# Optimization experiments

Hardware: AMD Instinct MI355X
Metric: run time of the kernel (lower is better)

Reference implementation:

```python
import jax, jax.numpy as jnp
import numpy as np

EMBED = 768
HEADS = 12


def setup_inputs() -> dict:
    key = jax.random.key(0)
    k1, k2, k3 = jax.random.split(key, 3)
    B, N, E = 2, 2048, EMBED
    x = jax.random.normal(k1, (B, N, E), dtype=jnp.float32)
    w_qkv = jax.random.normal(k2, (3 * E, E), dtype=jnp.float32) * (1.0 / np.sqrt(E))
    b_qkv = jnp.zeros((3 * E,), dtype=jnp.float32)
    w_o = jax.random.normal(k3, (E, E), dtype=jnp.float32) * (1.0 / np.sqrt(E))
    b_o = jnp.zeros((E,), dtype=jnp.float32)
    return {"x": x, "w_qkv": w_qkv, "b_qkv": b_qkv, "w_o": w_o, "b_o": b_o}


def reference(x, w_qkv, b_qkv, w_o, b_o):
    B, N, E = x.shape
    H = HEADS
    d = E // H
    # fused qkv projection (torch Linear: x @ W^T + b)
    qkv = x @ w_qkv.T + b_qkv                       # [B, N, 3E]
    # Rearrange 'b n (h qkv e) -> b qkv h n e'
    qkv = qkv.reshape(B, N, H, 3, d).transpose(0, 3, 2, 1, 4)  # [B, 3, H, N, d]
    q, k, v = qkv[:, 0], qkv[:, 1], qkv[:, 2]       # each [B, H, N, d]
    scores = jnp.einsum("bhqd,bhkd->bhqk", q, k)    # [B, H, N, N]
    attn = jax.nn.softmax(scores / jnp.sqrt(jnp.float32(E)), axis=-1)
    ctx = jnp.einsum("bhqk,bhkd->bhqd", attn, v)    # [B, H, N, d]
    ctx = ctx.transpose(0, 2, 1, 3).reshape(B, N, E)  # 'b h n d -> b n (h d)'
    out = ctx @ w_o.T + b_o
    return out
```

## Files before the change

### kernel.cpp

```cpp
#include <hip/hip_runtime.h>

#define BB 2
#define NN 2048
#define EE 768
#define HH 12
#define DD 64
#define MM (BB*NN)
#define E3 (3*EE)
#define NSPLIT 2
#define KEYS_PER_SPLIT (NN/NSPLIT)
#define QSCALE 0.05205877280961602f

typedef __bf16 bf16x8 __attribute__((ext_vector_type(8)));
typedef float  f32x4  __attribute__((ext_vector_type(4)));
typedef unsigned short u16x8 __attribute__((ext_vector_type(8)));

#define MFMA(a,b,c) __builtin_amdgcn_mfma_f32_16x16x32_bf16(a,b,c,0,0,0)

__device__ __forceinline__ unsigned short f2bf(float f) {
    unsigned int u = __float_as_uint(f);
    u += 0x7FFFu + ((u >> 16) & 1u);
    return (unsigned short)(u >> 16);
}

__device__ __forceinline__ bf16x8 as_bf16x8(u16x8 v) {
    union { u16x8 u; bf16x8 b; } c; c.u = v; return c.b;
}

typedef __attribute__((address_space(3))) unsigned int as3u32;
typedef __attribute__((address_space(1))) unsigned int as1u32;
__device__ __forceinline__ void gll16(const void* g, void* l) {
    __builtin_amdgcn_global_load_lds((const as1u32*)(uintptr_t)g,
                                     (as3u32*)(unsigned int)(uintptr_t)l, 16, 0, 0);
}

#define XB4 786432
#define WQ4 442368
#define WO4 147456
__global__ __launch_bounds__(256)
void cast3(const float* __restrict__ x, const float* __restrict__ wq,
           const float* __restrict__ wo, unsigned short* __restrict__ dst) {
    int i = blockIdx.x * 256 + threadIdx.x;
    const float* src;
    int off;
    if (i < XB4)            { src = x;  off = i; }
    else if (i < XB4+WQ4)   { src = wq; off = i - XB4; }
    else                    { src = wo; off = i - XB4 - WQ4; }
    float4 v = ((const float4*)src)[off];
    ushort4 o;
    o.x = f2bf(v.x); o.y = f2bf(v.y); o.z = f2bf(v.z); o.w = f2bf(v.w);
    ((ushort4*)dst)[i] = o;
}

__global__ __launch_bounds__(256)
void gemm_qkv(const unsigned short* __restrict__ A, const unsigned short* __restrict__ W,
              const float* __restrict__ bias,
              unsigned short* __restrict__ o0, unsigned short* __restrict__ o1,
              unsigned short* __restrict__ o2)
{
    __shared__ unsigned short As[2][128 * 32];
    __shared__ unsigned short Bs[2][64 * 32];

    const int tid = threadIdx.x;
    const int l = tid & 63;
    const int w = tid >> 6;
    const int m0 = blockIdx.x * 128;
    const int c0 = blockIdx.y * 64;
    const int wm = (w >> 1) * 64;
    const int wn = (w & 1) * 32;

    const unsigned short* s_src[3];
    int s_off[3]; bool s_isA[3];
    #pragma unroll
    for (int s = 0; s < 3; ++s) {
        const int ch = 3*w + s;
        if (ch < 8) {
            s_src[s] = A + (size_t)(m0 + ch*16 + (l>>2)) * EE + (l&3)*8;
            s_off[s] = ch*512; s_isA[s] = true;
        } else {
            s_src[s] = W + (size_t)(c0 + (ch-8)*16 + (l>>2)) * EE + (l&3)*8;
            s_off[s] = (ch-8)*512; s_isA[s] = false;
        }
    }

    const f32x4 zero4 = {0.f, 0.f, 0.f, 0.f};
    f32x4 acc[4][2];
    #pragma unroll
    for (int i = 0; i < 4; ++i)
        #pragma unroll
        for (int j = 0; j < 2; ++j) acc[i][j] = zero4;

    auto stage = [&](unsigned short* aB, unsigned short* bB, int k0) {
        #pragma unroll
        for (int s = 0; s < 3; ++s)
            gll16(s_src[s] + k0, (s_isA[s] ? aB : bB) + s_off[s]);
    };
    auto compute = [&](const unsigned short* aB, const unsigned short* bB) {
        bf16x8 af[4], bf[2];
        #pragma unroll
        for (int i = 0; i < 4; ++i)
            af[i] = *(const bf16x8*)&aB[(wm + 16*i + (l&15))*32 + (l>>4)*8];
        #pragma unroll
        for (int j = 0; j < 2; ++j)
            bf[j] = *(const bf16x8*)&bB[(wn + 16*j + (l&15))*32 + (l>>4)*8];
        #pragma unroll
        for (int i = 0; i < 4; ++i)
            #pragma unroll
            for (int j = 0; j < 2; ++j)
                acc[i][j] = MFMA(af[i], bf[j], acc[i][j]);
    };

    stage(As[0], Bs[0], 0);
    asm volatile("s_waitcnt vmcnt(0)" ::: "memory");
    __builtin_amdgcn_s_barrier();

    for (int k0 = 0; k0 < EE; k0 += 64) {
        stage(As[1], Bs[1], k0 + 32);
        compute(As[0], Bs[0]);
        asm volatile("s_waitcnt vmcnt(0)" ::: "memory");
        __builtin_amdgcn_s_barrier();
        if (k0 + 64 < EE) stage(As[0], Bs[0], k0 + 64);
        compute(As[1], Bs[1]);
        asm volatile("s_waitcnt vmcnt(0)" ::: "memory");
        __builtin_amdgcn_s_barrier();
    }

    const int sec = c0 >> 6;
    const int hh = sec / 3;
    const int tt = sec - hh*3;
    #pragma unroll
    for (int j = 0; j < 2; ++j) {
        const int col = c0 + wn + 16*j + (l&15);
        const int dcol = wn + 16*j + (l&15);
        const float bj = bias[col];
        #pragma unroll
        for (int i = 0; i < 4; ++i) {
            const int row0 = m0 + wm + 16*i + (l>>4)*4;
            const int b = row0 >> 11;
            const int n = row0 & (NN - 1);
            if (tt == 2) {
                ushort4 pk;
                pk.x = f2bf(acc[i][j][0] + bj);
                pk.y = f2bf(acc[i][j][1] + bj);
                pk.z = f2bf(acc[i][j][2] + bj);
                pk.w = f2bf(acc[i][j][3] + bj);
                *(ushort4*)&o2[(((size_t)b*HH + hh)*DD + dcol)*NN + n] = pk;
            } else {
                unsigned short* dst = (tt == 0) ? o0 : o1;
                #pragma unroll
                for (int r = 0; r < 4; ++r) {
                    float val = acc[i][j][r] + bj;
                    if (tt == 0) val *= QSCALE;
                    dst[(((size_t)b*HH + hh)*NN + n + r)*DD + dcol] = f2bf(val);
                }
            }
        }
    }
}

__global__ __launch_bounds__(256)
void gemm_out(const unsigned short* __restrict__ A, const unsigned short* __restrict__ W,
              const float* __restrict__ bias, float* __restrict__ of)
{
    __shared__ unsigned short As[2][64 * 32];
    __shared__ unsigned short Bs[2][64 * 32];

    const int tid = threadIdx.x;
    const int l = tid & 63;
    const int w = tid >> 6;
    const int m0 = blockIdx.x * 64;
    const int c0 = blockIdx.y * 64;
    const int wm = (w >> 1) * 32;
    const int wn = (w & 1) * 32;

    const unsigned short* s_src[2];
    int s_off[2]; bool s_isA[2];
    #pragma unroll
    for (int s = 0; s < 2; ++s) {
        const int ch = 2*w + s;
        if (ch < 4) {
            s_src[s] = A + (size_t)(m0 + ch*16 + (l>>2)) * EE + (l&3)*8;
            s_off[s] = ch*512; s_isA[s] = true;
        } else {
            s_src[s] = W + (size_t)(c0 + (ch-4)*16 + (l>>2)) * EE + (l&3)*8;
            s_off[s] = (ch-4)*512; s_isA[s] = false;
        }
    }

    const f32x4 zero4 = {0.f, 0.f, 0.f, 0.f};
    f32x4 acc[2][2];
    #pragma unroll
    for (int i = 0; i < 2; ++i)
        #pragma unroll
        for (int j = 0; j < 2; ++j) acc[i][j] = zero4;

    auto stage = [&](unsigned short* aB, unsigned short* bB, int k0) {
        #pragma unroll
        for (int s = 0; s < 2; ++s)
            gll16(s_src[s] + k0, (s_isA[s] ? aB : bB) + s_off[s]);
    };
    auto compute = [&](const unsigned short* aB, const unsigned short* bB) {
        bf16x8 af[2], bf[2];
        #pragma unroll
        for (int i = 0; i < 2; ++i)
            af[i] = *(const bf16x8*)&aB[(wm + 16*i + (l&15))*32 + (l>>4)*8];
        #pragma unroll
        for (int j = 0; j < 2; ++j)
            bf[j] = *(const bf16x8*)&bB[(wn + 16*j + (l&15))*32 + (l>>4)*8];
        #pragma unroll
        for (int i = 0; i < 2; ++i)
            #pragma unroll
            for (int j = 0; j < 2; ++j)
                acc[i][j] = MFMA(af[i], bf[j], acc[i][j]);
    };

    stage(As[0], Bs[0], 0);
    asm volatile("s_waitcnt vmcnt(0)" ::: "memory");
    __builtin_amdgcn_s_barrier();

    for (int k0 = 0; k0 < EE; k0 += 64) {
        stage(As[1], Bs[1], k0 + 32);
        compute(As[0], Bs[0]);
        asm volatile("s_waitcnt vmcnt(0)" ::: "memory");
        __builtin_amdgcn_s_barrier();
        if (k0 + 64 < EE) stage(As[0], Bs[0], k0 + 64);
        compute(As[1], Bs[1]);
        asm volatile("s_waitcnt vmcnt(0)" ::: "memory");
        __builtin_amdgcn_s_barrier();
    }

    #pragma unroll
    for (int j = 0; j < 2; ++j) {
        const int col = c0 + wn + 16*j + (l&15);
        const float bj = bias[col];
        #pragma unroll
        for (int i = 0; i < 2; ++i) {
            #pragma unroll
            for (int r = 0; r < 4; ++r) {
                const int row = m0 + wm + 16*i + (l>>4)*4 + r;
                of[(size_t)row * EE + col] = acc[i][j][r] + bj;
            }
        }
    }
}

struct KVT { u16x8 k0, k1, k2, k3, v0, v1, v2, v3; };

__global__ __launch_bounds__(256)
void attn_mfma(const unsigned short* __restrict__ Q, const unsigned short* __restrict__ K,
               const unsigned short* __restrict__ Vt_g,
               float* __restrict__ Opart, float* __restrict__ Lpart)
{
    __shared__ unsigned short Ks[2 * 64 * 64];
    __shared__ unsigned short Vt[2 * 64 * 64];

    const int tid = threadIdx.x;
    const int l = tid & 63;
    const int w = tid >> 6;
    const int quad = l >> 4;
    const int lc = l & 15;
    const int x7 = lc & 7;

    const int id = blockIdx.x;
    const int sp = blockIdx.y;
    const int bh = id % 24;
    const int bq = id / 24;
    const size_t hb = (size_t)bh * NN * DD;

    const f32x4 zero4 = {0.f, 0.f, 0.f, 0.f};

    const int qrow = bq*64 + w*16 + lc;
    const bf16x8 qf0 = *(const bf16x8*)(Q + hb + (size_t)qrow*DD +      quad*8);
    const bf16x8 qf1 = *(const bf16x8*)(Q + hb + (size_t)qrow*DD + 32 + quad*8);

    f32x4 o[4];
    #pragma unroll
    for (int dj = 0; dj < 4; ++dj) o[dj] = zero4;
    float lsum = 0.f;

    const int srow = tid >> 2;
    const int sc = tid & 3;
    const unsigned short* kbase = K + hb + (size_t)(sp*KEYS_PER_SPLIT + srow)*DD + sc*16;
    const int keyA = (sc & 1)*8 + (sc >> 1)*32;
    const unsigned short* vbase = Vt_g + hb + (size_t)srow*NN + sp*KEYS_PER_SPLIT + keyA;
    const int c0s = ((2*sc)     ^ (srow & 7)) * 8;
    const int c1s = ((2*sc + 1) ^ (srow & 7)) * 8;
    const int so = srow * 64;

    const int chq0 = ((    quad) ^ x7) * 8;
    const int chq1 = ((4 + quad) ^ x7) * 8;

    auto loadt = [&](KVT& R, int kt) {
        const unsigned short* k0p = kbase + (size_t)kt*128*DD;
        const unsigned short* v0p = vbase + kt*128;
        R.k0 = *(const u16x8*)k0p;
        R.k1 = *(const u16x8*)(k0p + 8);
        R.k2 = *(const u16x8*)(k0p + (size_t)64*DD);
        R.k3 = *(const u16x8*)(k0p + (size_t)64*DD + 8);
        R.v0 = *(const u16x8*)v0p;
        R.v1 = *(const u16x8*)(v0p + 16);
        R.v2 = *(const u16x8*)(v0p + 64);
        R.v3 = *(const u16x8*)(v0p + 64 + 16);
    };

    auto step = [&](KVT& CUR, KVT& NXT, int kt) {
        asm volatile("s_waitcnt lgkmcnt(0)" ::: "memory");
        __builtin_amdgcn_s_barrier();

        u16x8 w0 = __builtin_shufflevector(CUR.v0, CUR.v1, 0,1,2,3, 8,9,10,11);
        u16x8 w1 = __builtin_shufflevector(CUR.v0, CUR.v1, 4,5,6,7, 12,13,14,15);
        u16x8 w2 = __builtin_shufflevector(CUR.v2, CUR.v3, 0,1,2,3, 8,9,10,11);
        u16x8 w3 = __builtin_shufflevector(CUR.v2, CUR.v3, 4,5,6,7, 12,13,14,15);
        *(u16x8*)&Ks[so + c0s]        = CUR.k0;
        *(u16x8*)&Ks[so + c1s]        = CUR.k1;
        *(u16x8*)&Ks[4096 + so + c0s] = CUR.k2;
        *(u16x8*)&Ks[4096 + so + c1s] = CUR.k3;
        *(u16x8*)&Vt[so + c0s]        = w0;
        *(u16x8*)&Vt[so + c1s]        = w1;
        *(u16x8*)&Vt[4096 + so + c0s] = w2;
        *(u16x8*)&Vt[4096 + so + c1s] = w3;

        if (kt + 1 < KEYS_PER_SPLIT/128) loadt(NXT, kt + 1);

        asm volatile("s_waitcnt lgkmcnt(0)" ::: "memory");
        __builtin_amdgcn_s_barrier();
        __builtin_amdgcn_sched_barrier(0);

        #pragma unroll
        for (int hf = 0; hf < 2; ++hf) {
            const int base = hf * 4096;

            f32x4 st[4];
            #pragma unroll
            for (int jf = 0; jf < 4; ++jf) {
                bf16x8 kf0 = *(const bf16x8*)&Ks[base + (16*jf + lc)*64 + chq0];
                bf16x8 kf1 = *(const bf16x8*)&Ks[base + (16*jf + lc)*64 + chq1];
                f32x4 acc0 = MFMA(kf0, qf0, zero4);
                st[jf] = MFMA(kf1, qf1, acc0);
            }

            f32x4 ev[4];
            #pragma unroll
            for (int jf = 0; jf < 4; ++jf) {
                ev[jf][0] = __builtin_amdgcn_exp2f(st[jf][0]);
                ev[jf][1] = __builtin_amdgcn_exp2f(st[jf][1]);
                ev[jf][2] = __builtin_amdgcn_exp2f(st[jf][2]);
                ev[jf][3] = __builtin_amdgcn_exp2f(st[jf][3]);
                lsum += (ev[jf][0] + ev[jf][1]) + (ev[jf][2] + ev[jf][3]);
            }
            u16x8 p0, p1;
            #pragma unroll
            for (int r = 0; r < 4; ++r) {
                p0[r]     = f2bf(ev[0][r]);
                p0[r + 4] = f2bf(ev[1][r]);
                p1[r]     = f2bf(ev[2][r]);
                p1[r + 4] = f2bf(ev[3][r]);
            }
            const bf16x8 pf0 = as_bf16x8(p0);
            const bf16x8 pf1 = as_bf16x8(p1);

            #pragma unroll
            for (int dj = 0; dj < 4; ++dj) {
                bf16x8 vf0 = *(const bf16x8*)&Vt[base + (16*dj + lc)*64 + chq0];
                bf16x8 vf1 = *(const bf16x8*)&Vt[base + (16*dj + lc)*64 + chq1];
                o[dj] = MFMA(vf0, pf0, o[dj]);
                o[dj] = MFMA(vf1, pf1, o[dj]);
            }
        }
    };

    KVT ra, rb;
    loadt(ra, 0);
    for (int it = 0; it < KEYS_PER_SPLIT/256; ++it) {
        step(ra, rb, 2*it);
        step(rb, ra, 2*it + 1);
    }

    lsum += __shfl_xor(lsum, 16);
    lsum += __shfl_xor(lsum, 32);

    const int n = bq*64 + w*16 + lc;
    float* op = Opart + ((size_t)(sp*24 + bh)*NN + n)*DD + quad*4;
    #pragma unroll
    for (int dj = 0; dj < 4; ++dj)
        *(f32x4*)(op + 16*dj) = o[dj];
    if (quad == 0)
        Lpart[(size_t)(sp*24 + bh)*NN + n] = lsum;
}

#define RTOT (24*NN)
__global__ __launch_bounds__(256)
void combine(const float* __restrict__ Op, const float* __restrict__ Lp,
             unsigned short* __restrict__ ctx)
{
    const int t = blockIdx.x * 256 + threadIdx.x;
    const int r = t >> 4;
    const int c = t & 15;
    const float4 a = *(const float4*)&Op[(size_t)r*DD + c*4];
    const float4 bv = *(const float4*)&Op[((size_t)RTOT + r)*DD + c*4];
    const float inv = 1.f / (Lp[r] + Lp[RTOT + r]);
    const int bh = r >> 11;
    const int n = r & (NN - 1);
    const int b = bh / 12;
    const int h = bh - b*12;
    ushort4 pk;
    pk.x = f2bf((a.x + bv.x) * inv);
    pk.y = f2bf((a.y + bv.y) * inv);
    pk.z = f2bf((a.z + bv.z) * inv);
    pk.w = f2bf((a.w + bv.w) * inv);
    *(ushort4*)&ctx[((size_t)(b*NN + n))*EE + h*DD + c*4] = pk;
}

extern "C" void kernel_launch(void* const* d_in, const int* in_sizes, int n_in,
                              void* d_out, int out_size, void* d_ws, size_t ws_size,
                              hipStream_t stream)
{
    const float* x     = (const float*)d_in[0];
    const float* w_qkv = (const float*)d_in[1];
    const float* b_qkv = (const float*)d_in[2];
    const float* w_o   = (const float*)d_in[3];
    const float* b_o   = (const float*)d_in[4];
    float* out = (float*)d_out;

    unsigned short* wsu = (unsigned short*)d_ws;
    const size_t XB = (size_t)MM * EE;
    const size_t WQ = (size_t)E3 * EE;
    const size_t WO = (size_t)EE * EE;
    const size_t HS = (size_t)BB * HH * NN * DD;
    unsigned short* xb   = wsu;
    unsigned short* wqb  = xb  + XB;
    unsigned short* wob  = wqb + WQ;
    unsigned short* qb   = wob + WO;
    unsigned short* kb   = qb  + HS;
    unsigned short* vtb  = kb  + HS;
    unsigned short* ctxb = vtb + HS;
    float* opart = (float*)(ctxb + HS);
    float* lpart = opart + (size_t)NSPLIT * 24 * NN * DD;

    cast3<<<(XB4 + WQ4 + WO4)/256, 256, 0, stream>>>(x, w_qkv, w_o, xb);

    dim3 g1(MM/128, E3/64);
    gemm_qkv<<<g1, 256, 0, stream>>>(xb, wqb, b_qkv, qb, kb, vtb);

    dim3 g2(768, NSPLIT);
    attn_mfma<<<g2, 256, 0, stream>>>(qb, kb, vtb, opart, lpart);

    combine<<<(RTOT*16)/256, 256, 0, stream>>>(opart, lpart, ctxb);

    dim3 g3(MM/64, EE/64);
    gemm_out<<<g3, 256, 0, stream>>>(ctxb, wob, b_o, out);
}
```

Baseline: 171.4 us.

## Load K and V fragments directly from global memory, dropping LDS staging

The attention kernel no longer stages K and V tiles through shared memory with double-buffered register prefetch and barriers. Each wave now reads its MFMA operand fragments straight from global memory (8-byte loads for V^T), assembles the V operand from four 4-element pieces, and drops all block-level synchronisation. This removes LDS traffic and barrier stalls, but each wave redundantly fetches the same K/V data through cache with smaller, less coalesced loads and no explicit prefetch overlap.

```diff
diff --git a/kernel.cpp b/kernel.cpp
--- a/kernel.cpp
+++ b/kernel.cpp
@@ -14,6 +14,7 @@
 typedef __bf16 bf16x8 __attribute__((ext_vector_type(8)));
 typedef float  f32x4  __attribute__((ext_vector_type(4)));
 typedef unsigned short u16x8 __attribute__((ext_vector_type(8)));
+typedef unsigned short u16x4 __attribute__((ext_vector_type(4)));
 
 #define MFMA(a,b,c) __builtin_amdgcn_mfma_f32_16x16x32_bf16(a,b,c,0,0,0)
 
@@ -25,6 +26,10 @@
 
 __device__ __forceinline__ bf16x8 as_bf16x8(u16x8 v) {
     union { u16x8 u; bf16x8 b; } c; c.u = v; return c.b;
+}
+
+__device__ __forceinline__ bf16x8 combine48(u16x4 a, u16x4 b) {
+    union { u16x4 q[2]; bf16x8 v; } c; c.q[0] = a; c.q[1] = b; return c.v;
 }
 
 typedef __attribute__((address_space(3))) unsigned int as3u32;
@@ -244,22 +249,16 @@
     }
 }
 
-struct KVT { u16x8 k0, k1, k2, k3, v0, v1, v2, v3; };
-
 __global__ __launch_bounds__(256)
 void attn_mfma(const unsigned short* __restrict__ Q, const unsigned short* __restrict__ K,
                const unsigned short* __restrict__ Vt_g,
                float* __restrict__ Opart, float* __restrict__ Lpart)
 {
-    __shared__ unsigned short Ks[2 * 64 * 64];
-    __shared__ unsigned short Vt[2 * 64 * 64];
-
     const int tid = threadIdx.x;
     const int l = tid & 63;
     const int w = tid >> 6;
     const int quad = l >> 4;
     const int lc = l & 15;
-    const int x7 = lc & 7;
 
     const int id = blockIdx.x;
     const int sp = blockIdx.y;
@@ -278,102 +277,57 @@
     for (int dj = 0; dj < 4; ++dj) o[dj] = zero4;
     float lsum = 0.f;
 
-    const int srow = tid >> 2;
-    const int sc = tid & 3;
-    const unsigned short* kbase = K + hb + (size_t)(sp*KEYS_PER_SPLIT + srow)*DD + sc*16;
-    const int keyA = (sc & 1)*8 + (sc >> 1)*32;
-    const unsigned short* vbase = Vt_g + hb + (size_t)srow*NN + sp*KEYS_PER_SPLIT + keyA;
-    const int c0s = ((2*sc)     ^ (srow & 7)) * 8;
-    const int c1s = ((2*sc + 1) ^ (srow & 7)) * 8;
-    const int so = srow * 64;
-
-    const int chq0 = ((    quad) ^ x7) * 8;
-    const int chq1 = ((4 + quad) ^ x7) * 8;
-
-    auto loadt = [&](KVT& R, int kt) {
-        const unsigned short* k0p = kbase + (size_t)kt*128*DD;
-        const unsigned short* v0p = vbase + kt*128;
-        R.k0 = *(const u16x8*)k0p;
-        R.k1 = *(const u16x8*)(k0p + 8);
-        R.k2 = *(const u16x8*)(k0p + (size_t)64*DD);
-        R.k3 = *(const u16x8*)(k0p + (size_t)64*DD + 8);
-        R.v0 = *(const u16x8*)v0p;
-        R.v1 = *(const u16x8*)(v0p + 16);
-        R.v2 = *(const u16x8*)(v0p + 64);
-        R.v3 = *(const u16x8*)(v0p + 64 + 16);
-    };
-
-    auto step = [&](KVT& CUR, KVT& NXT, int kt) {
-        asm volatile("s_waitcnt lgkmcnt(0)" ::: "memory");
-        __builtin_amdgcn_s_barrier();
-
-        u16x8 w0 = __builtin_shufflevector(CUR.v0, CUR.v1, 0,1,2,3, 8,9,10,11);
-        u16x8 w1 = __builtin_shufflevector(CUR.v0, CUR.v1, 4,5,6,7, 12,13,14,15);
-        u16x8 w2 = __builtin_shufflevector(CUR.v2, CUR.v3, 0,1,2,3, 8,9,10,11);
-        u16x8 w3 = __builtin_shufflevector(CUR.v2, CUR.v3, 4,5,6,7, 12,13,14,15);
-        *(u16x8*)&Ks[so + c0s]        = CUR.k0;
-        *(u16x8*)&Ks[so + c1s]        = CUR.k1;
-        *(u16x8*)&Ks[4096 + so + c0s] = CUR.k2;
-        *(u16x8*)&Ks[4096 + so + c1s] = CUR.k3;
-        *(u16x8*)&Vt[so + c0s]        = w0;
-        *(u16x8*)&Vt[so + c1s]        = w1;
-        *(u16x8*)&Vt[4096 + so + c0s] = w2;
-        *(u16x8*)&Vt[4096 + so + c1s] = w3;
-
-        if (kt + 1 < KEYS_PER_SPLIT/128) loadt(NXT, kt + 1);
-
-        asm volatile("s_waitcnt lgkmcnt(0)" ::: "memory");
-        __builtin_amdgcn_s_barrier();
-        __builtin_amdgcn_sched_barrier(0);
-
-        #pragma unroll
-        for (int hf = 0; hf < 2; ++hf) {
-            const int base = hf * 4096;
-
-            f32x4 st[4];
-            #pragma unroll
-            for (int jf = 0; jf < 4; ++jf) {
-                bf16x8 kf0 = *(const bf16x8*)&Ks[base + (16*jf + lc)*64 + chq0];
-                bf16x8 kf1 = *(const bf16x8*)&Ks[base + (16*jf + lc)*64 + chq1];
-                f32x4 acc0 = MFMA(kf0, qf0, zero4);
-                st[jf] = MFMA(kf1, qf1, acc0);
-            }
-
-            f32x4 ev[4];
-            #pragma unroll
-            for (int jf = 0; jf < 4; ++jf) {
-                ev[jf][0] = __builtin_amdgcn_exp2f(st[jf][0]);
-                ev[jf][1] = __builtin_amdgcn_exp2f(st[jf][1]);
-                ev[jf][2] = __builtin_amdgcn_exp2f(st[jf][2]);
-                ev[jf][3] = __builtin_amdgcn_exp2f(st[jf][3]);
-                lsum += (ev[jf][0] + ev[jf][1]) + (ev[jf][2] + ev[jf][3]);
-            }
-            u16x8 p0, p1;
-            #pragma unroll
-            for (int r = 0; r < 4; ++r) {
-                p0[r]     = f2bf(ev[0][r]);
-                p0[r + 4] = f2bf(ev[1][r]);
-                p1[r]     = f2bf(ev[2][r]);
-                p1[r + 4] = f2bf(ev[3][r]);
-            }
-            const bf16x8 pf0 = as_bf16x8(p0);
-            const bf16x8 pf1 = as_bf16x8(p1);
-
-            #pragma unroll
-            for (int dj = 0; dj < 4; ++dj) {
-                bf16x8 vf0 = *(const bf16x8*)&Vt[base + (16*dj + lc)*64 + chq0];
-                bf16x8 vf1 = *(const bf16x8*)&Vt[base + (16*dj + lc)*64 + chq1];
-                o[dj] = MFMA(vf0, pf0, o[dj]);
-                o[dj] = MFMA(vf1, pf1, o[dj]);
-            }
-        }
-    };
-
-    KVT ra, rb;
-    loadt(ra, 0);
-    for (int it = 0; it < KEYS_PER_SPLIT/256; ++it) {
-        step(ra, rb, 2*it);
-        step(rb, ra, 2*it + 1);
+    const unsigned short* Kb = K + hb + (size_t)sp*KEYS_PER_SPLIT*DD;
+    const unsigned short* Vb = Vt_g + hb + sp*KEYS_PER_SPLIT;
+
+    for (int kt = 0; kt < KEYS_PER_SPLIT/64; ++kt) {
+        const int k64 = kt*64;
+
+        bf16x8 kf0[4], kf1[4];
+        #pragma unroll
+        for (int jf = 0; jf < 4; ++jf) {
+            const unsigned short* kp = Kb + (size_t)(k64 + 16*jf + lc)*DD + quad*8;
+            kf0[jf] = *(const bf16x8*)kp;
+            kf1[jf] = *(const bf16x8*)(kp + 32);
+        }
+
+        f32x4 st[4];
+        #pragma unroll
+        for (int jf = 0; jf < 4; ++jf) {
+            f32x4 acc0 = MFMA(kf0[jf], qf0, zero4);
+            st[jf] = MFMA(kf1[jf], qf1, acc0);
+        }
+
+        f32x4 ev[4];
+        #pragma unroll
+        for (int jf = 0; jf < 4; ++jf) {
+            ev[jf][0] = __builtin_amdgcn_exp2f(st[jf][0]);
+            ev[jf][1] = __builtin_amdgcn_exp2f(st[jf][1]);
+            ev[jf][2] = __builtin_amdgcn_exp2f(st[jf][2]);
+            ev[jf][3] = __builtin_amdgcn_exp2f(st[jf][3]);
+            lsum += (ev[jf][0] + ev[jf][1]) + (ev[jf][2] + ev[jf][3]);
+        }
+        u16x8 p0, p1;
+        #pragma unroll
+        for (int r = 0; r < 4; ++r) {
+            p0[r]     = f2bf(ev[0][r]);
+            p0[r + 4] = f2bf(ev[1][r]);
+            p1[r]     = f2bf(ev[2][r]);
+            p1[r + 4] = f2bf(ev[3][r]);
+        }
+        const bf16x8 pf0 = as_bf16x8(p0);
+        const bf16x8 pf1 = as_bf16x8(p1);
+
+        #pragma unroll
+        for (int dj = 0; dj < 4; ++dj) {
+            const unsigned short* vrow = Vb + (size_t)(16*dj + lc)*NN + k64 + 4*quad;
+            u16x4 a0 = *(const u16x4*)vrow;
+            u16x4 a1 = *(const u16x4*)(vrow + 16);
+            u16x4 a2 = *(const u16x4*)(vrow + 32);
+            u16x4 a3 = *(const u16x4*)(vrow + 48);
+            o[dj] = MFMA(combine48(a0, a1), pf0, o[dj]);
+            o[dj] = MFMA(combine48(a2, a3), pf1, o[dj]);
+        }
     }
 
     lsum += __shfl_xor(lsum, 16);
```

New measurement: 379.0 us. 121% more time.
